# Kernel optimization log

Hardware: AMD Instinct MI355X
Metric: run time of the kernel (lower is better)

The kernel has to match this reference:

```python
import jax, jax.numpy as jnp
import numpy as np

NEG_BIG = -9e15  # matches -9000000000000000.0 in the torch source
ALPHA = 0.2      # LeakyReLU negative slope


def setup_inputs() -> dict:
    key = jax.random.key(0)
    k1, k2, k3, k4 = jax.random.split(key, 4)
    N, F_in, F_out = 8192, 256, 128
    x = jax.random.normal(k1, (N, F_in), dtype=jnp.float32)
    adj = jax.random.randint(k2, (N, N), 0, 2, dtype=jnp.int32)
    W = jax.random.normal(k3, (F_in, F_out), dtype=jnp.float32) * 0.05
    a = jax.random.normal(k4, (2 * F_out, 1), dtype=jnp.float32) * 0.05
    return {"x": x, "adj": adj, "W": W, "a": a}


def reference(x, adj, W, a):
    # h = x @ W : [N, F]
    h = x @ W
    F_out = W.shape[1]
    # Algebraically identical to the concat formulation:
    # a^T [h_i || h_j] = h_i @ a1 + h_j @ a2
    a1 = a[:F_out, 0]
    a2 = a[F_out:, 0]
    src = h @ a1  # [N]
    dst = h @ a2  # [N]
    e = jax.nn.leaky_relu(src[:, None] + dst[None, :], negative_slope=ALPHA)  # [N, N]
    attention = jnp.where(adj > 0, e, NEG_BIG)
    attention = jax.nn.softmax(attention, axis=1)
    # dropout is identity in eval mode (training=False)
    h_prime = attention @ h  # [N, F]
    return h_prime
```

## Files before the change

kernel.cpp:

```cpp
#include <hip/hip_runtime.h>
#include <cstdint>

#define N 8192
#define FIN 256
#define FOUT 128
#define ALPHA 0.2f
#define KS 8
#define JSL (N / KS)
#define NSTEP (JSL / 32)

typedef unsigned short u16;
typedef __attribute__((ext_vector_type(8))) short short8;
typedef __attribute__((ext_vector_type(4))) float floatx4;

__device__ __forceinline__ u16 bf16_rne(float f) {
  uint32_t u = __float_as_uint(f);
  u += 0x7fff + ((u >> 16) & 1);
  return (u16)(u >> 16);
}

__global__ __launch_bounds__(256) void k_proj(const float* __restrict__ x,
                                              const float* __restrict__ W,
                                              const float* __restrict__ a,
                                              u16* __restrict__ hT3,
                                              float* __restrict__ srcv,
                                              float* __restrict__ dstv) {
  __shared__ float xs[8 * FIN];
  __shared__ float partS[4][4], partD[4][4];
  const int t = threadIdx.x;
  const int R0 = blockIdx.x * 8;

  const float4* xv = (const float4*)(x + (size_t)R0 * FIN);
  float4* xsv = (float4*)xs;
  xsv[t] = xv[t];
  xsv[t + 256] = xv[t + 256];
  __syncthreads();

  const int c  = t & 127;
  const int rg = (t >> 7) * 4;

  float acc[4] = {0.f, 0.f, 0.f, 0.f};
  float wa[4], wb[4];
  #pragma unroll
  for (int j = 0; j < 4; ++j) wa[j] = W[j * FOUT + c];
  #pragma unroll
  for (int j = 0; j < 4; ++j) wb[j] = W[(4 + j) * FOUT + c];

  for (int k4 = 0; k4 < FIN / 4; ++k4) {
    float wc[4];
    #pragma unroll
    for (int j = 0; j < 4; ++j) { wc[j] = wa[j]; wa[j] = wb[j]; }
    const int kn = (k4 + 2 < FIN / 4) ? k4 + 2 : k4;
    #pragma unroll
    for (int j = 0; j < 4; ++j) wb[j] = W[(kn * 4 + j) * FOUT + c];
    #pragma unroll
    for (int i = 0; i < 4; ++i) {
      const float4 xq = *(const float4*)&xs[(rg + i) * FIN + k4 * 4];
      acc[i] += xq.x * wc[0] + xq.y * wc[1] + xq.z * wc[2] + xq.w * wc[3];
    }
  }

  {
    const int j = R0 + rg;
    const int jb = j >> 5, q = (j >> 3) & 3, jj = j & 7;
    const int m = c & 15, nt = c >> 4;
    union { u16 u[4]; uint2 v; } pk;
    #pragma unroll
    for (int i = 0; i < 4; ++i) pk.u[i] = bf16_rne(acc[i]);
    *(uint2*)(hT3 + (size_t)(((jb * 8 + nt) * 64) + (m * 4 + q)) * 8 + jj) = pk.v;
  }

  const float a1 = a[c], a2 = a[FOUT + c];
  float s4[4], d4[4];
  #pragma unroll
  for (int i = 0; i < 4; ++i) { s4[i] = acc[i] * a1; d4[i] = acc[i] * a2; }
  #pragma unroll
  for (int off = 32; off > 0; off >>= 1) {
    #pragma unroll
    for (int i = 0; i < 4; ++i) {
      s4[i] += __shfl_down(s4[i], off);
      d4[i] += __shfl_down(d4[i], off);
    }
  }
  const int wv = t >> 6, lane = t & 63;
  if (lane == 0) {
    #pragma unroll
    for (int i = 0; i < 4; ++i) { partS[wv][i] = s4[i]; partD[wv][i] = d4[i]; }
  }
  __syncthreads();
  if (t < 16) {
    const int i = t & 3, rg2 = (t >> 2) & 1, which = t >> 3;
    if (which == 0) srcv[R0 + rg2 * 4 + i] = partS[rg2*2][i] + partS[rg2*2+1][i];
    else            dstv[R0 + rg2 * 4 + i] = partD[rg2*2][i] + partD[rg2*2+1][i];
  }
}

__global__ __launch_bounds__(256, 3) void k_gat(const int* __restrict__ adj,
                                                const u16* __restrict__ hT3,
                                                const float* __restrict__ srcv,
                                                const float* __restrict__ dstv,
                                                float* __restrict__ P,
                                                float* __restrict__ lp) {
  __shared__ float redP[2][16 * FOUT];
  __shared__ float redL[2][16];
  const int t = threadIdx.x;
  const int wv = t >> 6, lane = t & 63;
  const int q = lane >> 4, m = lane & 15;
  const int bm = blockIdx.x & 255;
  const int jp = blockIdx.x >> 8;
  const int sp = wv >> 1;
  const int jh = wv & 1;
  const int R0 = (bm * 2 + sp) * 16;
  const int j0 = (jp * 2 + jh) * JSL;

  const float srcm = srcv[R0 + m];
  const int*   adjp = adj + (size_t)(R0 + m) * N + j0 + q * 8;
  const float* dstp = dstv + j0 + q * 8;
  const u16*   hpl  = hT3 + (size_t)(j0 >> 5) * 4096 + (size_t)(m * 4 + q) * 8;

  floatx4 acc[8];
  #pragma unroll
  for (int nt = 0; nt < 8; ++nt) acc[nt] = (floatx4){0.f, 0.f, 0.f, 0.f};
  float lsum = 0.f;

  int4   aA0 = *(const int4*)(adjp),        aA1 = *(const int4*)(adjp + 4);
  float4 dA0 = *(const float4*)(dstp),      dA1 = *(const float4*)(dstp + 4);
  int4   aB0 = *(const int4*)(adjp + 32),   aB1 = *(const int4*)(adjp + 36);
  float4 dB0 = *(const float4*)(dstp + 32), dB1 = *(const float4*)(dstp + 36);

  #define GAT_STEP(I, A0_, A1_, D0_, D1_, NX)                                  \
  {                                                                            \
                                         \
    const u16* hpi = hpl + (size_t)(I) * 4096;                                 \
    short8 bf0 = *(const short8*)(hpi);                                        \
    short8 bf1 = *(const short8*)(hpi + 512);                                  \
    short8 bf2 = *(const short8*)(hpi + 1024);                                 \
    short8 bf3 = *(const short8*)(hpi + 1536);                                 \
    short8 bf4 = *(const short8*)(hpi + 2048);                                 \
    short8 bf5 = *(const short8*)(hpi + 2560);                                 \
    short8 bf6 = *(const short8*)(hpi + 3072);                                 \
    short8 bf7 = *(const short8*)(hpi + 3584);                                 \
    const int4   cA0 = A0_, cA1 = A1_;                                         \
    const float4 cD0 = D0_, cD1 = D1_;                                         \
                                      \
    A0_ = *(const int4*)(adjp + (NX) * 32);                                    \
    A1_ = *(const int4*)(adjp + (NX) * 32 + 4);                                \
    D0_ = *(const float4*)(dstp + (NX) * 32);                                  \
    D1_ = *(const float4*)(dstp + (NX) * 32 + 4);                              \
                                                            \
    const int   ai[8] = {cA0.x, cA0.y, cA0.z, cA0.w, cA1.x, cA1.y, cA1.z, cA1.w}; \
    const float df[8] = {cD0.x, cD0.y, cD0.z, cD0.w, cD1.x, cD1.y, cD1.z, cD1.w}; \
    union { u16 u[8]; short8 s; } pk;                                          \
    _Pragma("unroll")                                                          \
    for (int e = 0; e < 8; ++e) {                                              \
      float v = srcm + df[e];                                                  \
      v = fmaxf(v, ALPHA * v);                                                 \
      const float p = ai[e] > 0 ? __expf(v) : 0.f;                             \
      lsum += p;                                                               \
      pk.u[e] = bf16_rne(p);                                                   \
    }                                                                          \
                                                                \
    acc[0] = __builtin_amdgcn_mfma_f32_16x16x32_bf16(pk.s, bf0, acc[0], 0, 0, 0); \
    acc[1] = __builtin_amdgcn_mfma_f32_16x16x32_bf16(pk.s, bf1, acc[1], 0, 0, 0); \
    acc[2] = __builtin_amdgcn_mfma_f32_16x16x32_bf16(pk.s, bf2, acc[2], 0, 0, 0); \
    acc[3] = __builtin_amdgcn_mfma_f32_16x16x32_bf16(pk.s, bf3, acc[3], 0, 0, 0); \
    acc[4] = __builtin_amdgcn_mfma_f32_16x16x32_bf16(pk.s, bf4, acc[4], 0, 0, 0); \
    acc[5] = __builtin_amdgcn_mfma_f32_16x16x32_bf16(pk.s, bf5, acc[5], 0, 0, 0); \
    acc[6] = __builtin_amdgcn_mfma_f32_16x16x32_bf16(pk.s, bf6, acc[6], 0, 0, 0); \
    acc[7] = __builtin_amdgcn_mfma_f32_16x16x32_bf16(pk.s, bf7, acc[7], 0, 0, 0); \
  }

  for (int i = 0; i < NSTEP; i += 2) {
    const int nxA = (i + 2 < NSTEP) ? i + 2 : i;
    GAT_STEP(i, aA0, aA1, dA0, dA1, nxA)
    const int nxB = (i + 3 < NSTEP) ? i + 3 : i + 1;
    GAT_STEP(i + 1, aB0, aB1, dB0, dB1, nxB)
  }
  #undef GAT_STEP

  lsum += __shfl_xor(lsum, 16);
  lsum += __shfl_xor(lsum, 32);

  if (jh == 1) {
    float* rp = redP[sp];
    #pragma unroll
    for (int nt = 0; nt < 8; ++nt)
      #pragma unroll
      for (int ri = 0; ri < 4; ++ri)
        rp[(q * 4 + ri) * FOUT + nt * 16 + m] = acc[nt][ri];
    if (lane < 16) redL[sp][lane] = lsum;
  }
  __syncthreads();
  if (jh == 0) {
    const float* rp = redP[sp];
    float* Pp = P + ((size_t)jp * N + R0) * FOUT;
    #pragma unroll
    for (int nt = 0; nt < 8; ++nt)
      #pragma unroll
      for (int ri = 0; ri < 4; ++ri) {
        const int idx = (q * 4 + ri) * FOUT + nt * 16 + m;
        Pp[idx] = acc[nt][ri] + rp[idx];
      }
    if (lane < 16) lp[(size_t)jp * N + R0 + lane] = lsum + redL[sp][lane];
  }
}

__global__ __launch_bounds__(256) void k_norm(const float* __restrict__ P,
                                              const float* __restrict__ lp,
                                              float* __restrict__ out) {
  const int idx = blockIdx.x * 256 + threadIdx.x;
  const int rr = idx >> 5;
  const int c4 = (idx & 31) * 4;
  const float l = lp[rr] + lp[N + rr] + lp[2 * N + rr] + lp[3 * N + rr];
  const float inv = 1.0f / l;
  float4 s = {0.f, 0.f, 0.f, 0.f};
  #pragma unroll
  for (int jp = 0; jp < 4; ++jp) {
    const float4 p = *(const float4*)(P + ((size_t)jp * N + rr) * FOUT + c4);
    s.x += p.x; s.y += p.y; s.z += p.z; s.w += p.w;
  }
  s.x *= inv; s.y *= inv; s.z *= inv; s.w *= inv;
  *(float4*)(out + (size_t)rr * FOUT + c4) = s;
}

extern "C" void kernel_launch(void* const* d_in, const int* in_sizes, int n_in,
                              void* d_out, int out_size, void* d_ws, size_t ws_size,
                              hipStream_t stream) {
  const float* x   = (const float*)d_in[0];
  const int*   adj = (const int*)d_in[1];
  const float* W   = (const float*)d_in[2];
  const float* a   = (const float*)d_in[3];
  float* out = (float*)d_out;

  char* ws = (char*)d_ws;
  u16*   hT3  = (u16*)ws;     ws += (size_t)FOUT * N * sizeof(u16);
  float* srcv = (float*)ws;   ws += (size_t)N * sizeof(float);
  float* dstv = (float*)ws;   ws += (size_t)N * sizeof(float);
  float* P    = (float*)ws;   ws += (size_t)4 * N * FOUT * sizeof(float);
  float* lp   = (float*)ws;   ws += (size_t)4 * N * sizeof(float);

  k_proj<<<N / 8, 256, 0, stream>>>(x, W, a, hT3, srcv, dstv);
  k_gat <<<1024, 256, 0, stream>>>(adj, hT3, srcv, dstv, P, lp);
  k_norm<<<(N * FOUT / 4) / 256, 256, 0, stream>>>(P, lp, out);
}
```

Before: 476.4 us.

## Give each wave a full j-slice and deepen adjacency prefetch to four steps

Each k_gat wave now owns a distinct 16-row tile over a 2048-column j slice, replacing the pair of waves that split the slice and then reduced partial accumulators through LDS with a barrier. The grid drops from 1024 to 512 blocks. The adj/dst prefetch is deepened from two to four steps in flight, and the occupancy hint is lowered from 3 to 2 blocks per SIMD to make room for the extra registers. This removes the LDS reduction and the sync but halves the number of blocks, which may reduce latency hiding on the memory-bound adj stream.

New measurement: 495.2 us. +4.0%, slower.

```diff
diff --git a/kernel.cpp b/kernel.cpp
--- a/kernel.cpp
+++ b/kernel.cpp
@@ -5,8 +5,8 @@
 #define FIN 256
 #define FOUT 128
 #define ALPHA 0.2f
-#define KS 8
-#define JSL (N / KS)
+#define JP 4
+#define JSL (N / JP)
 #define NSTEP (JSL / 32)
 
 typedef unsigned short u16;
@@ -95,23 +95,19 @@
   }
 }
 
-__global__ __launch_bounds__(256, 3) void k_gat(const int* __restrict__ adj,
+__global__ __launch_bounds__(256, 2) void k_gat(const int* __restrict__ adj,
                                                 const u16* __restrict__ hT3,
                                                 const float* __restrict__ srcv,
                                                 const float* __restrict__ dstv,
                                                 float* __restrict__ P,
                                                 float* __restrict__ lp) {
-  __shared__ float redP[2][16 * FOUT];
-  __shared__ float redL[2][16];
   const int t = threadIdx.x;
   const int wv = t >> 6, lane = t & 63;
   const int q = lane >> 4, m = lane & 15;
-  const int bm = blockIdx.x & 255;
-  const int jp = blockIdx.x >> 8;
-  const int sp = wv >> 1;
-  const int jh = wv & 1;
-  const int R0 = (bm * 2 + sp) * 16;
-  const int j0 = (jp * 2 + jh) * JSL;
+  const int bm = blockIdx.x & 127;
+  const int jp = blockIdx.x >> 7;
+  const int R0 = (bm * 4 + wv) * 16;
+  const int j0 = jp * JSL;
 
   const float srcm = srcv[R0 + m];
   const int*   adjp = adj + (size_t)(R0 + m) * N + j0 + q * 8;
@@ -127,10 +123,14 @@
   float4 dA0 = *(const float4*)(dstp),      dA1 = *(const float4*)(dstp + 4);
   int4   aB0 = *(const int4*)(adjp + 32),   aB1 = *(const int4*)(adjp + 36);
   float4 dB0 = *(const float4*)(dstp + 32), dB1 = *(const float4*)(dstp + 36);
+  int4   aC0 = *(const int4*)(adjp + 64),   aC1 = *(const int4*)(adjp + 68);
+  float4 dC0 = *(const float4*)(dstp + 64), dC1 = *(const float4*)(dstp + 68);
+  int4   aD0 = *(const int4*)(adjp + 96),   aD1 = *(const int4*)(adjp + 100);
+  float4 dD0 = *(const float4*)(dstp + 96), dD1 = *(const float4*)(dstp + 100);
 
   #define GAT_STEP(I, A0_, A1_, D0_, D1_, NX)                                  \
   {                                                                            \
-                                         \
+          \
     const u16* hpi = hpl + (size_t)(I) * 4096;                                 \
     short8 bf0 = *(const short8*)(hpi);                                        \
     short8 bf1 = *(const short8*)(hpi + 512);                                  \
@@ -170,39 +170,28 @@
     acc[7] = __builtin_amdgcn_mfma_f32_16x16x32_bf16(pk.s, bf7, acc[7], 0, 0, 0); \
   }
 
-  for (int i = 0; i < NSTEP; i += 2) {
-    const int nxA = (i + 2 < NSTEP) ? i + 2 : i;
+  for (int i = 0; i < NSTEP; i += 4) {
+    const int nxA = (i + 4 < NSTEP) ? i + 4 : i;
     GAT_STEP(i, aA0, aA1, dA0, dA1, nxA)
-    const int nxB = (i + 3 < NSTEP) ? i + 3 : i + 1;
+    const int nxB = (i + 5 < NSTEP) ? i + 5 : i + 1;
     GAT_STEP(i + 1, aB0, aB1, dB0, dB1, nxB)
+    const int nxC = (i + 6 < NSTEP) ? i + 6 : i + 2;
+    GAT_STEP(i + 2, aC0, aC1, dC0, dC1, nxC)
+    const int nxD = (i + 7 < NSTEP) ? i + 7 : i + 3;
+    GAT_STEP(i + 3, aD0, aD1, dD0, dD1, nxD)
   }
   #undef GAT_STEP
 
   lsum += __shfl_xor(lsum, 16);
   lsum += __shfl_xor(lsum, 32);
-
-  if (jh == 1) {
-    float* rp = redP[sp];
-    #pragma unroll
-    for (int nt = 0; nt < 8; ++nt)
-      #pragma unroll
-      for (int ri = 0; ri < 4; ++ri)
-        rp[(q * 4 + ri) * FOUT + nt * 16 + m] = acc[nt][ri];
-    if (lane < 16) redL[sp][lane] = lsum;
-  }
-  __syncthreads();
-  if (jh == 0) {
-    const float* rp = redP[sp];
-    float* Pp = P + ((size_t)jp * N + R0) * FOUT;
-    #pragma unroll
-    for (int nt = 0; nt < 8; ++nt)
-      #pragma unroll
-      for (int ri = 0; ri < 4; ++ri) {
-        const int idx = (q * 4 + ri) * FOUT + nt * 16 + m;
-        Pp[idx] = acc[nt][ri] + rp[idx];
-      }
-    if (lane < 16) lp[(size_t)jp * N + R0 + lane] = lsum + redL[sp][lane];
-  }
+  if (lane < 16) lp[(size_t)jp * N + R0 + lane] = lsum;
+
+  float* Pp = P + ((size_t)jp * N + R0) * FOUT;
+  #pragma unroll
+  for (int nt = 0; nt < 8; ++nt)
+    #pragma unroll
+    for (int ri = 0; ri < 4; ++ri)
+      Pp[(size_t)(q * 4 + ri) * FOUT + nt * 16 + m] = acc[nt][ri];
 }
 
 __global__ __launch_bounds__(256) void k_norm(const float* __restrict__ P,
@@ -236,10 +225,10 @@
   u16*   hT3  = (u16*)ws;     ws += (size_t)FOUT * N * sizeof(u16);
   float* srcv = (float*)ws;   ws += (size_t)N * sizeof(float);
   float* dstv = (float*)ws;   ws += (size_t)N * sizeof(float);
-  float* P    = (float*)ws;   ws += (size_t)4 * N * FOUT * sizeof(float);
-  float* lp   = (float*)ws;   ws += (size_t)4 * N * sizeof(float);
+  float* P    = (float*)ws;   ws += (size_t)JP * N * FOUT * sizeof(float);
+  float* lp   = (float*)ws;   ws += (size_t)JP * N * sizeof(float);
 
   k_proj<<<N / 8, 256, 0, stream>>>(x, W, a, hT3, srcv, dstv);
-  k_gat <<<1024, 256, 0, stream>>>(adj, hT3, srcv, dstv, P, lp);
+  k_gat <<<128 * JP, 256, 0, stream>>>(adj, hT3, srcv, dstv, P, lp);
   k_norm<<<(N * FOUT / 4) / 256, 256, 0, stream>>>(P, lp, out);
 }
```
